# Kernel optimization log

Hardware: AMD Instinct MI355X
Metric: run time of the kernel (lower is better)

The kernel has to match this reference:

```python
import jax, jax.numpy as jnp
import numpy as np

B, S, HID = 1, 2048, 2048
H, KVH, D = 16, 8, 128
N_REP = H // KVH
SCALING = float(np.sqrt(D))  # head_dim ** 0.5 (nGPT uses positive exponent)
SQK_INIT_VALUE = 1.0
SQK_INIT_SCALING = 0.02
EPS = 1e-8


def _rotate_half(x):
    x1, x2 = jnp.split(x, 2, axis=-1)
    return jnp.concatenate((-x2, x1), axis=-1)


def setup_inputs() -> dict:
    key = jax.random.key(0)
    ks = jax.random.split(key, 8)
    hidden_states = jax.random.normal(ks[0], (B, S, HID), dtype=jnp.float32)
    # realistic RoPE tables, full rotary (rotary_dim == head_dim)
    inv_freq = 1.0 / (10000.0 ** (np.arange(0, D, 2, dtype=np.float32) / D))
    t = np.arange(S, dtype=np.float32)
    freqs = np.outer(t, inv_freq)                      # [S, D/2]
    emb = np.concatenate([freqs, freqs], axis=-1)      # [S, D]
    cos = jnp.asarray(np.cos(emb))[None].repeat(B, 0)  # [B, S, D]
    sin = jnp.asarray(np.sin(emb))[None].repeat(B, 0)
    # additive causal mask [B, 1, S, S]
    causal = jnp.tril(jnp.ones((S, S), dtype=bool))
    attention_mask = jnp.where(causal, 0.0, jnp.finfo(jnp.float32).min)[None, None].repeat(B, 0)
    sd = 0.02
    Wq = jax.random.normal(ks[1], (H * D, HID), dtype=jnp.float32) * sd
    Wk = jax.random.normal(ks[2], (KVH * D, HID), dtype=jnp.float32) * sd
    Wv = jax.random.normal(ks[3], (KVH * D, HID), dtype=jnp.float32) * sd
    Wo = jax.random.normal(ks[4], (HID, H * D), dtype=jnp.float32) * sd
    sqk_w = jnp.full((H * D,), SQK_INIT_SCALING, dtype=jnp.float32)  # Linear(1, H*D) weight, init constant
    return {"hidden_states": hidden_states, "cos": cos, "sin": sin,
            "attention_mask": attention_mask, "Wq": Wq, "Wk": Wk, "Wv": Wv,
            "Wo": Wo, "sqk_w": sqk_w}


def _l2_normalize(x):
    return x / (jnp.linalg.norm(x, axis=-1, keepdims=True) + EPS)


def reference(hidden_states, cos, sin, attention_mask, Wq, Wk, Wv, Wo, sqk_w):
    b, s, _ = hidden_states.shape
    # projections (torch Linear: y = x @ W.T)
    q = jnp.einsum('bsd,ed->bse', hidden_states, Wq).reshape(b, s, H, D).transpose(0, 2, 1, 3)
    k = jnp.einsum('bsd,ed->bse', hidden_states, Wk).reshape(b, s, KVH, D).transpose(0, 2, 1, 3)
    v = jnp.einsum('bsd,ed->bse', hidden_states, Wv).reshape(b, s, KVH, D).transpose(0, 2, 1, 3)
    # RoPE, cos/sin broadcast over heads: [B,1,S,D]
    c, sn = cos[:, None], sin[:, None]
    q = q * c + _rotate_half(q) * sn
    k = k * c + _rotate_half(k) * sn
    # nGPT: L2-normalize q,k; learnable per-channel scale on q
    sqk = (sqk_w * (SQK_INIT_VALUE / SQK_INIT_SCALING)).reshape(1, H, 1, D)
    q = _l2_normalize(q) * sqk ** 2
    k = _l2_normalize(k)
    # GQA: repeat kv heads
    k = jnp.repeat(k, N_REP, axis=1)
    v = jnp.repeat(v, N_REP, axis=1)
    scores = jnp.einsum('bhqd,bhkd->bhqk', q, k) * SCALING
    scores = scores + attention_mask
    attn = jax.nn.softmax(scores.astype(jnp.float32), axis=-1).astype(q.dtype)
    out = jnp.einsum('bhqk,bhkd->bhqd', attn, v)
    out = out.transpose(0, 2, 1, 3).reshape(b, s, H * D)
    return jnp.einsum('bse,de->bsd', out, Wo)
```

## Files before the change

### kernel.cpp

```cpp
#include <hip/hip_runtime.h>

typedef unsigned short u16;
typedef __attribute__((ext_vector_type(4))) float f32x4;
typedef __attribute__((ext_vector_type(16))) float f32x16;
typedef __attribute__((ext_vector_type(8))) __bf16 bf16x8;
typedef __attribute__((ext_vector_type(8))) u16 u16x8;
typedef __attribute__((ext_vector_type(4))) u16 u16x4;
typedef __attribute__((ext_vector_type(4))) unsigned int u32x4;

#define S_LEN 2048
#define NH 16
#define NKV 8
#define QSCALE_LOG2E 16.322118857f
#define M2INIT 16.6f
#define EXP2(x) __builtin_amdgcn_exp2f(x)

#define SWZK(r) (((((r) & 7) << 4)) ^ (((((r) >> 3) & 1)) << 7))
#define SWZV(r) (((((r) & 7) << 4)) ^ (((((r) >> 3) & 1)) << 6))

#define AS1(p) ((const __attribute__((address_space(1))) void*)(p))
#define AS3(p) ((__attribute__((address_space(3))) void*)(p))

#define PIPE_WAIT6() asm volatile("s_waitcnt vmcnt(6)\ns_barrier" ::: "memory")
#define PIPE_WAIT0() asm volatile("s_waitcnt vmcnt(0)\ns_barrier" ::: "memory")

__device__ __forceinline__ float b2f(u16 u) {
    return __uint_as_float(((unsigned int)u) << 16);
}
__device__ __forceinline__ u16 f2b(float f) {
    unsigned int x = __float_as_uint(f);
    unsigned int r = (x + 0x7FFFu + ((x >> 16) & 1u)) >> 16;
    return (u16)r;
}

__global__ __launch_bounds__(256) void cast_all(const float* __restrict__ hs,
                                                const float* __restrict__ Wq,
                                                const float* __restrict__ Wk,
                                                const float* __restrict__ Wv,
                                                const float* __restrict__ Wo,
                                                u16* __restrict__ hsb,
                                                u16* __restrict__ wcat,
                                                u16* __restrict__ wob) {
    int i = blockIdx.x * 256 + threadIdx.x;
    const float* src; u16* dst; int off;
    if (i < 1048576)      { src = hs; dst = hsb;            off = i; }
    else if (i < 2097152) { src = Wq; dst = wcat;           off = i - 1048576; }
    else if (i < 2621440) { src = Wk; dst = wcat + 4194304; off = i - 2097152; }
    else if (i < 3145728) { src = Wv; dst = wcat + 6291456; off = i - 2621440; }
    else                  { src = Wo; dst = wob;            off = i - 3145728; }
    f32x4 v = reinterpret_cast<const f32x4*>(src)[off];
    u16x4 o;
    o[0] = f2b(v[0]); o[1] = f2b(v[1]); o[2] = f2b(v[2]); o[3] = f2b(v[3]);
    reinterpret_cast<u16x4*>(dst)[off] = o;
}

__global__ __launch_bounds__(512) void gemm_qkv(const u16* __restrict__ A,
                                                const u16* __restrict__ B,
                                                const float* __restrict__ cosb,
                                                const float* __restrict__ sinb,
                                                const float* __restrict__ sqkw,
                                                u16* __restrict__ qb,
                                                u16* __restrict__ kb,
                                                u16* __restrict__ vt) {
    const int K = 2048;
    __shared__ alignas(16) u16 As[3][128 * 64];
    __shared__ alignas(16) u16 Bs[3][256 * 64];
    int tid = threadIdx.x, lane = tid & 63, wave = tid >> 6;
    int row0 = blockIdx.y * 128, col0 = blockIdx.x * 256;
    int wr = (wave >> 1) * 32;
    int wc = (wave & 1) * 128;
    int l15 = lane & 15, lg = lane >> 4;

    f32x4 acc[2][8] = {};

    auto stage = [&](int bf, int k0) {
#pragma unroll
        for (int i = 0; i < 2; i++) {
            int slot = i * 8 + wave;
            int r = slot * 8 + (lane >> 3);
            int c = (lane & 7) ^ (r & 7);
            __builtin_amdgcn_global_load_lds(AS1(A + (size_t)(row0 + r) * K + k0 + c * 8),
                                             AS3(&As[bf][slot * 512]), 16, 0, 0);
        }
#pragma unroll
        for (int i = 0; i < 4; i++) {
            int slot = i * 8 + wave;
            int r = slot * 8 + (lane >> 3);
            int c = (lane & 7) ^ (r & 7);
            __builtin_amdgcn_global_load_lds(AS1(B + (size_t)(col0 + r) * K + k0 + c * 8),
                                             AS3(&Bs[bf][slot * 512]), 16, 0, 0);
        }
    };

    const int nk = K >> 6;
    stage(0, 0);
    stage(1, 64);

    for (int t = 0; t < nk; ++t) {
        int buf = t % 3;
        __builtin_amdgcn_sched_barrier(0);
        if (t + 1 < nk) PIPE_WAIT6(); else PIPE_WAIT0();
        if (t + 2 < nk) stage((t + 2) % 3, (t + 2) * 64);

        __builtin_amdgcn_s_setprio(1);
#pragma unroll
        for (int kk = 0; kk < 2; kk++) {
            bf16x8 af[2], bg[8];
#pragma unroll
            for (int m = 0; m < 2; m++) {
                int r = wr + m * 16 + l15;
                af[m] = *reinterpret_cast<const bf16x8*>(&As[buf][r * 64 + (((kk * 4 + lg) ^ (r & 7)) * 8)]);
            }
#pragma unroll
            for (int n = 0; n < 8; n++) {
                int r = wc + n * 16 + l15;
                bg[n] = *reinterpret_cast<const bf16x8*>(&Bs[buf][r * 64 + (((kk * 4 + lg) ^ (r & 7)) * 8)]);
            }
#pragma unroll
            for (int m = 0; m < 2; m++)
#pragma unroll
                for (int n = 0; n < 8; n++)
                    acc[m][n] = __builtin_amdgcn_mfma_f32_16x16x32_bf16(af[m], bg[n], acc[m][n], 0, 0, 0);
        }
        __builtin_amdgcn_s_setprio(0);
    }

    int c32 = blockIdx.x * 2 + (wave & 1);
    if (c32 < 24) {
        bool isQ = c32 < 16;
        float w2[8];
        if (isQ) {
#pragma unroll
            for (int j = 0; j < 8; j++) {
                float w = sqkw[c32 * 128 + j * 16 + l15] * 50.f;
                w2[j] = w * w * QSCALE_LOG2E;
            }
        }
        u16* outb = isQ ? (qb + (size_t)c32 * S_LEN * 128)
                        : (kb + (size_t)(c32 - 16) * S_LEN * 128);
#pragma unroll
        for (int m = 0; m < 2; m++)
#pragma unroll
            for (int r = 0; r < 4; r++) {
                int s = row0 + wr + m * 16 + lg * 4 + r;
                const float* crow = cosb + (size_t)s * 128;
                const float* srow = sinb + (size_t)s * 128;
                float y[8];
                float ss = 0.f;
#pragma unroll
                for (int j = 0; j < 4; j++) {
                    float c  = crow[j * 16 + l15];
                    float sn = srow[j * 16 + l15];
                    float x0 = acc[m][j][r], x1 = acc[m][j + 4][r];
                    float a = x0 * c - x1 * sn;
                    float b = x1 * c + x0 * sn;
                    y[j] = a; y[j + 4] = b;
                    ss += a * a + b * b;
                }
                ss += __shfl_xor(ss, 1);
                ss += __shfl_xor(ss, 2);
                ss += __shfl_xor(ss, 4);
                ss += __shfl_xor(ss, 8);
                float inv = 1.f / (sqrtf(ss) + 1e-8f);
                u16* orow = outb + (size_t)s * 128;
                if (isQ) {
#pragma unroll
                    for (int j = 0; j < 8; j++)
                        orow[j * 16 + l15] = f2b(y[j] * inv * w2[j]);
                } else {
#pragma unroll
                    for (int j = 0; j < 8; j++)
                        orow[j * 16 + l15] = f2b(y[j] * inv);
                }
            }
    } else {
        int g = c32 - 24;
#pragma unroll
        for (int n = 0; n < 8; n++) {
            int d = n * 16 + l15;
            u16* vrow = vt + (size_t)(g * 128 + d) * S_LEN;
#pragma unroll
            for (int m = 0; m < 2; m++) {
                u16x4 pk;
#pragma unroll
                for (int r = 0; r < 4; r++) pk[r] = f2b(acc[m][n][r]);
                *reinterpret_cast<u16x4*>(&vrow[row0 + wr + m * 16 + lg * 4]) = pk;
            }
        }
    }
}

__global__ __launch_bounds__(256) void gemm_o(const u16* __restrict__ A,
                                              const u16* __restrict__ B,
                                              float* __restrict__ C,
                                              int M, int N, int K) {
    __shared__ alignas(16) u16 As[3][128 * 64];
    __shared__ alignas(16) u16 Bs[3][64 * 64];
    int tid = threadIdx.x, lane = tid & 63, wave = tid >> 6;
    int row0 = blockIdx.y * 128, col0 = blockIdx.x * 64;
    int wr = wave * 32;
    int l15 = lane & 15, lg = lane >> 4;

    f32x4 acc[2][4] = {};

    auto stage = [&](int bf, int k0) {
#pragma unroll
        for (int i = 0; i < 4; i++) {
            int slot = i * 4 + wave;
            int r = slot * 8 + (lane >> 3);
            int c = (lane & 7) ^ (r & 7);
            __builtin_amdgcn_global_load_lds(AS1(A + (size_t)(row0 + r) * K + k0 + c * 8),
                                             AS3(&As[bf][slot * 512]), 16, 0, 0);
        }
#pragma unroll
        for (int i = 0; i < 2; i++) {
            int slot = i * 4 + wave;
            int r = slot * 8 + (lane >> 3);
            int c = (lane & 7) ^ (r & 7);
            __builtin_amdgcn_global_load_lds(AS1(B + (size_t)(col0 + r) * K + k0 + c * 8),
                                             AS3(&Bs[bf][slot * 512]), 16, 0, 0);
        }
    };

    const int nk = K >> 6;
    stage(0, 0);
    stage(1, 64);

    for (int t = 0; t < nk; ++t) {
        int buf = t % 3;
        __builtin_amdgcn_sched_barrier(0);
        if (t + 1 < nk) PIPE_WAIT6(); else PIPE_WAIT0();
        if (t + 2 < nk) stage((t + 2) % 3, (t + 2) * 64);

        __builtin_amdgcn_s_setprio(1);
#pragma unroll
        for (int kk = 0; kk < 2; kk++) {
            bf16x8 af[2], bg[4];
#pragma unroll
            for (int m = 0; m < 2; m++) {
                int r = wr + m * 16 + l15;
                af[m] = *reinterpret_cast<const bf16x8*>(&As[buf][r * 64 + (((kk * 4 + lg) ^ (r & 7)) * 8)]);
            }
#pragma unroll
            for (int n = 0; n < 4; n++) {
                int r = n * 16 + l15;
                bg[n] = *reinterpret_cast<const bf16x8*>(&Bs[buf][r * 64 + (((kk * 4 + lg) ^ (r & 7)) * 8)]);
            }
#pragma unroll
            for (int m = 0; m < 2; m++)
#pragma unroll
                for (int n = 0; n < 4; n++)
                    acc[m][n] = __builtin_amdgcn_mfma_f32_16x16x32_bf16(af[m], bg[n], acc[m][n], 0, 0, 0);
        }
        __builtin_amdgcn_s_setprio(0);
    }

#pragma unroll
    for (int m = 0; m < 2; m++)
#pragma unroll
        for (int n = 0; n < 4; n++)
#pragma unroll
            for (int r = 0; r < 4; r++) {
                int row = row0 + wr + m * 16 + lg * 4 + r;
                int col = col0 + n * 16 + l15;
                C[(size_t)row * N + col] = acc[m][n][r];
            }
}

__global__ __launch_bounds__(256) void attn_mfma(const u16* __restrict__ Qb,
                                                 const u16* __restrict__ Kb,
                                                 const u16* __restrict__ Vt,
                                                 u16* __restrict__ Ao) {
    __shared__ alignas(16) char smem[50432];
    u16* Ks = (u16*)smem;
    u16* Vs = (u16*)(smem + 16384);
    float* scrO = (float*)smem;
    float* scrL = (float*)(smem + 32768);
    u16*   scrT = (u16*)(smem + 33024);

    int tid = threadIdx.x, lane = tid & 63, wv = tid >> 6;
    int b = blockIdx.x;
    int xcd = b & 7, j = b >> 3;
    int g = xcd;
    int h = xcd * 2 + (j & 1);
    int z = j >> 1;
    int qi = (z < 16) ? (31 - z) : (z - 16);
    int qb0 = qi * 64;
    int l31 = lane & 31, hi = lane >> 5;
    int qoff = (wv >> 1) * 32, koff = (wv & 1) * 32;
    int qabs = qb0 + qoff + l31;

    bf16x8 qf[8];
    {
        const u16* qrow = Qb + ((size_t)h * S_LEN + qabs) * 128;
#pragma unroll
        for (int kd = 0; kd < 8; kd++)
            qf[kd] = *reinterpret_cast<const bf16x8*>(qrow + kd * 16 + hi * 8);
    }

    const u16* kbase = Kb + (size_t)g * S_LEN * 128;
    const u16* vbase = Vt + (size_t)g * 128 * S_LEN;

    int rk = wv * 16 + (lane >> 4);
    int ck = lane & 15;
    int rv = wv * 32 + (lane >> 3);
    int cv = lane & 7;

    u16x8 kreg[4], vreg[4];
    f32x16 oacc[4] = {};
    float lpart = 0.f;

    int nt = qi + 1;

#pragma unroll
    for (int i = 0; i < 4; i++) {
        kreg[i] = *reinterpret_cast<const u16x8*>(kbase + (size_t)(rk + 4 * i) * 128 + ck * 8);
        vreg[i] = *reinterpret_cast<const u16x8*>(vbase + (size_t)(rv + 8 * i) * S_LEN + cv * 8);
    }

    for (int t = 0; t < nt; ++t) {
        int k0 = t * 64;
        __syncthreads();
#pragma unroll
        for (int i = 0; i < 4; i++) {
            int r = rk + 4 * i;
            *reinterpret_cast<u16x8*>((char*)Ks + r * 256 + ((ck * 16) ^ SWZK(r))) = kreg[i];
            int r2 = rv + 8 * i;
            *reinterpret_cast<u16x8*>((char*)Vs + r2 * 128 + ((cv * 16) ^ SWZV(r2))) = vreg[i];
        }
        __syncthreads();

        if (t + 1 < nt) {
            int kn = k0 + 64;
#pragma unroll
            for (int i = 0; i < 4; i++) {
                kreg[i] = *reinterpret_cast<const u16x8*>(kbase + (size_t)(kn + rk + 4 * i) * 128 + ck * 8);
                vreg[i] = *reinterpret_cast<const u16x8*>(vbase + (size_t)(rv + 8 * i) * S_LEN + kn + cv * 8);
            }
        }

        f32x16 s0 = {}, s1 = {};
        int krow = koff + l31;
        char* krp = (char*)Ks + krow * 256;
        int ksw = SWZK(krow);
        __builtin_amdgcn_s_setprio(1);
#pragma unroll
        for (int kd = 0; kd < 8; kd += 2) {
            bf16x8 kf0 = *reinterpret_cast<const bf16x8*>(krp + ((kd * 32 + hi * 16) ^ ksw));
            bf16x8 kf1 = *reinterpret_cast<const bf16x8*>(krp + (((kd + 1) * 32 + hi * 16) ^ ksw));
            s0 = __builtin_amdgcn_mfma_f32_32x32x16_bf16(kf0, qf[kd], s0, 0, 0, 0);
            s1 = __builtin_amdgcn_mfma_f32_32x32x16_bf16(kf1, qf[kd + 1], s1, 0, 0, 0);
        }
        __builtin_amdgcn_s_setprio(0);

        float p[16];
        bool maskt = (t == nt - 1);
#pragma unroll
        for (int r = 0; r < 16; r++) {
            float s = s0[r] + s1[r];
            if (maskt) {
                int key = k0 + koff + (r & 3) + 8 * (r >> 2) + 4 * hi;
                if (key > qabs) s = -1e30f;
            }
            float pv = EXP2(s - M2INIT);
            p[r] = pv;
            lpart += pv;
        }

        bf16x8 pf[2];
#pragma unroll
        for (int ks = 0; ks < 2; ks++) {
            int bb = ks * 8;
            unsigned int A0 = (unsigned int)f2b(p[bb + 0]) | ((unsigned int)f2b(p[bb + 1]) << 16);
            unsigned int A1 = (unsigned int)f2b(p[bb + 2]) | ((unsigned int)f2b(p[bb + 3]) << 16);
            unsigned int A2 = (unsigned int)f2b(p[bb + 4]) | ((unsigned int)f2b(p[bb + 5]) << 16);
            unsigned int A3 = (unsigned int)f2b(p[bb + 6]) | ((unsigned int)f2b(p[bb + 7]) << 16);
            unsigned int S0 = __shfl_xor(A0, 32);
            unsigned int S1 = __shfl_xor(A1, 32);
            unsigned int S2 = __shfl_xor(A2, 32);
            unsigned int S3 = __shfl_xor(A3, 32);
            u32x4 w;
            w[0] = hi ? S2 : A0;
            w[1] = hi ? S3 : A1;
            w[2] = hi ? A2 : S0;
            w[3] = hi ? A3 : S1;
            pf[ks] = *reinterpret_cast<bf16x8*>(&w);
        }

        __builtin_amdgcn_s_setprio(1);
#pragma unroll
        for (int db = 0; db < 4; db++) {
            int vr = db * 32 + l31;
            char* vrp = (char*)Vs + vr * 128;
            int vsw = SWZV(vr);
#pragma unroll
            for (int ks = 0; ks < 2; ks++) {
                bf16x8 vf = *reinterpret_cast<const bf16x8*>(vrp + ((koff * 2 + ks * 32 + hi * 16) ^ vsw));
                oacc[db] = __builtin_amdgcn_mfma_f32_32x32x16_bf16(vf, pf[ks], oacc[db], 0, 0, 0);
            }
        }
        __builtin_amdgcn_s_setprio(0);
    }

    float lw = lpart + __shfl_xor(lpart, 32);
    int rg = wv >> 1;
    __syncthreads();
    if (wv & 1) {
#pragma unroll
        for (int db = 0; db < 4; db++)
#pragma unroll
            for (int r = 0; r < 16; r++) {
                int d = db * 32 + (r & 3) + 8 * (r >> 2) + 4 * hi;
                scrO[(rg * 128 + d) * 32 + l31] = oacc[db][r];
            }
        if (lane < 32) scrL[rg * 32 + l31] = lw;
    }
    __syncthreads();
    if (!(wv & 1)) {
        float inv = 1.f / (lw + scrL[rg * 32 + l31]);
#pragma unroll
        for (int db = 0; db < 4; db++)
#pragma unroll
            for (int r = 0; r < 16; r++) {
                int d = db * 32 + (r & 3) + 8 * (r >> 2) + 4 * hi;
                float o = (oacc[db][r] + scrO[(rg * 128 + d) * 32 + l31]) * inv;
                scrT[(rg * 32 + l31) * 136 + d] = f2b(o);
            }
    }
    __syncthreads();
    for (int i = tid; i < 64 * 16; i += 256) {
        int q = i >> 4, c = i & 15;
        u16x8 v = *reinterpret_cast<const u16x8*>(&scrT[q * 136 + c * 8]);
        *reinterpret_cast<u16x8*>(&Ao[(size_t)(qb0 + q) * 2048 + h * 128 + c * 8]) = v;
    }
}

extern "C" void kernel_launch(void* const* d_in, const int* in_sizes, int n_in,
                              void* d_out, int out_size, void* d_ws, size_t ws_size,
                              hipStream_t stream) {
    const float* hs   = (const float*)d_in[0];
    const float* cosb = (const float*)d_in[1];
    const float* sinb = (const float*)d_in[2];
    const float* Wq   = (const float*)d_in[4];
    const float* Wk   = (const float*)d_in[5];
    const float* Wv   = (const float*)d_in[6];
    const float* Wo   = (const float*)d_in[7];
    const float* sqkw = (const float*)d_in[8];

    char* ws = (char*)d_ws;
    u16*   hsb  = (u16*)(ws);
    u16*   wcat = (u16*)(ws + 8388608);
    u16*   wob  = (u16*)(ws + 25165824);
    u16*   qb   = (u16*)(ws + 33554432);
    u16*   kb   = (u16*)(ws + 41943040);
    u16*   vt   = (u16*)(ws + 46137344);
    u16*   ao   = (u16*)(ws + 50331648);

    cast_all<<<16384, 256, 0, stream>>>(hs, Wq, Wk, Wv, Wo, hsb, wcat, wob);

    gemm_qkv<<<dim3(16, 16), 512, 0, stream>>>(hsb, wcat, cosb, sinb, sqkw, qb, kb, vt);

    attn_mfma<<<512, 256, 0, stream>>>(qb, kb, vt, ao);

    gemm_o<<<dim3(32, 16), 256, 0, stream>>>(ao, wob, (float*)d_out, 2048, 2048, 2048);
}
```

Measured before the change: 145.0 us.

## Interleave LDS reads, MFMA phases and global prefetch in QKV GEMM loop

Restructures the QKV projection GEMM main loop into four phases per k-tile. Each phase loads a slice of B fragments from LDS and issues part of the next tile's global-to-LDS prefetch, then runs a small MFMA batch, with barriers and lgkmcnt waits between phases. The aim is to spread the memory traffic across the MFMA work, in the style of a ping-pong schedule, instead of issuing all prefetches up front. The extra barriers per tile could add synchronisation overhead.

```diff
diff --git a/kernel.cpp b/kernel.cpp
--- a/kernel.cpp
+++ b/kernel.cpp
@@ -23,6 +23,8 @@
 
 #define PIPE_WAIT6() asm volatile("s_waitcnt vmcnt(6)\ns_barrier" ::: "memory")
 #define PIPE_WAIT0() asm volatile("s_waitcnt vmcnt(0)\ns_barrier" ::: "memory")
+#define LGKM0() do { asm volatile("s_waitcnt lgkmcnt(0)" ::: "memory"); \
+                     __builtin_amdgcn_sched_barrier(0); } while (0)
 
 __device__ __forceinline__ float b2f(u16 u) {
     return __uint_as_float(((unsigned int)u) << 16);
@@ -98,31 +100,86 @@
 
     for (int t = 0; t < nk; ++t) {
         int buf = t % 3;
+        bool pre = (t + 2 < nk);
+        int bf2 = (t + 2) % 3;
+        int k2 = (t + 2) * 64;
         __builtin_amdgcn_sched_barrier(0);
         if (t + 1 < nk) PIPE_WAIT6(); else PIPE_WAIT0();
-        if (t + 2 < nk) stage((t + 2) % 3, (t + 2) * 64);
-
+
+        bf16x8 af[2][2], bq[2][2];
+
+#pragma unroll
+        for (int m = 0; m < 2; m++) {
+            int r = wr + m * 16 + l15;
+#pragma unroll
+            for (int kk = 0; kk < 2; kk++)
+                af[m][kk] = *reinterpret_cast<const bf16x8*>(&As[buf][r * 64 + (((kk * 4 + lg) ^ (r & 7)) * 8)]);
+        }
+#pragma unroll
+        for (int nn = 0; nn < 2; nn++) {
+            int r = wc + nn * 16 + l15;
+#pragma unroll
+            for (int kk = 0; kk < 2; kk++)
+                bq[nn][kk] = *reinterpret_cast<const bf16x8*>(&Bs[buf][r * 64 + (((kk * 4 + lg) ^ (r & 7)) * 8)]);
+        }
+        if (pre) {
+#pragma unroll
+            for (int i = 0; i < 2; i++) {
+                int slot = i * 8 + wave;
+                int r = slot * 8 + (lane >> 3);
+                int c = (lane & 7) ^ (r & 7);
+                __builtin_amdgcn_global_load_lds(AS1(A + (size_t)(row0 + r) * K + k2 + c * 8),
+                                                 AS3(&As[bf2][slot * 512]), 16, 0, 0);
+            }
+        }
+        __builtin_amdgcn_s_barrier();
+        LGKM0();
         __builtin_amdgcn_s_setprio(1);
 #pragma unroll
-        for (int kk = 0; kk < 2; kk++) {
-            bf16x8 af[2], bg[8];
-#pragma unroll
-            for (int m = 0; m < 2; m++) {
-                int r = wr + m * 16 + l15;
-                af[m] = *reinterpret_cast<const bf16x8*>(&As[buf][r * 64 + (((kk * 4 + lg) ^ (r & 7)) * 8)]);
-            }
-#pragma unroll
-            for (int n = 0; n < 8; n++) {
-                int r = wc + n * 16 + l15;
-                bg[n] = *reinterpret_cast<const bf16x8*>(&Bs[buf][r * 64 + (((kk * 4 + lg) ^ (r & 7)) * 8)]);
-            }
+        for (int m = 0; m < 2; m++)
+#pragma unroll
+            for (int nn = 0; nn < 2; nn++)
+#pragma unroll
+                for (int kk = 0; kk < 2; kk++)
+                    acc[m][nn] = __builtin_amdgcn_mfma_f32_16x16x32_bf16(af[m][kk], bq[nn][kk], acc[m][nn], 0, 0, 0);
+        __builtin_amdgcn_s_setprio(0);
+        __builtin_amdgcn_s_barrier();
+        __builtin_amdgcn_sched_barrier(0);
+
+#pragma unroll
+        for (int p = 1; p < 4; p++) {
+#pragma unroll
+            for (int nn = 0; nn < 2; nn++) {
+                int r = wc + (p * 2 + nn) * 16 + l15;
+#pragma unroll
+                for (int kk = 0; kk < 2; kk++)
+                    bq[nn][kk] = *reinterpret_cast<const bf16x8*>(&Bs[buf][r * 64 + (((kk * 4 + lg) ^ (r & 7)) * 8)]);
+            }
+            if (pre && p < 3) {
+#pragma unroll
+                for (int j = 0; j < 2; j++) {
+                    int i = (p - 1) * 2 + j;
+                    int slot = i * 8 + wave;
+                    int r = slot * 8 + (lane >> 3);
+                    int c = (lane & 7) ^ (r & 7);
+                    __builtin_amdgcn_global_load_lds(AS1(B + (size_t)(col0 + r) * K + k2 + c * 8),
+                                                     AS3(&Bs[bf2][slot * 512]), 16, 0, 0);
+                }
+            }
+            __builtin_amdgcn_s_barrier();
+            LGKM0();
+            __builtin_amdgcn_s_setprio(1);
 #pragma unroll
             for (int m = 0; m < 2; m++)
 #pragma unroll
-                for (int n = 0; n < 8; n++)
-                    acc[m][n] = __builtin_amdgcn_mfma_f32_16x16x32_bf16(af[m], bg[n], acc[m][n], 0, 0, 0);
-        }
-        __builtin_amdgcn_s_setprio(0);
+                for (int nn = 0; nn < 2; nn++)
+#pragma unroll
+                    for (int kk = 0; kk < 2; kk++)
+                        acc[m][p * 2 + nn] = __builtin_amdgcn_mfma_f32_16x16x32_bf16(af[m][kk], bq[nn][kk], acc[m][p * 2 + nn], 0, 0, 0);
+            __builtin_amdgcn_s_setprio(0);
+            __builtin_amdgcn_s_barrier();
+            __builtin_amdgcn_sched_barrier(0);
+        }
     }
 
     int c32 = blockIdx.x * 2 + (wave & 1);
```

After: 144.6 us. No clear change (-0.3%).
